# Kernel optimization log

Hardware: AMD Instinct MI355X
Metric: run time of the kernel (lower is better)

The kernel has to match this reference:

```python
import jax, jax.numpy as jnp
import numpy as np

N = 100000      # nodes
E = 1600000     # edges (avg degree 16)
IN_DIM = 256
HID = 128
EPS = 0.3


def setup_inputs() -> dict:
    key = jax.random.key(0)
    ks = jax.random.split(key, 6)
    x = jax.random.normal(ks[0], (N, IN_DIM), dtype=jnp.float32)
    # edges without self-loops (dst = src + nonzero offset mod N)
    src = jax.random.randint(ks[1], (E,), 0, N)
    off = jax.random.randint(ks[2], (E,), 1, N)
    dst = (src + off) % N
    edge_index = jnp.stack([src, dst]).astype(jnp.int32)
    # xavier_normal_ with gain=1.414 for t1 and gate
    g1 = 1.414 * np.sqrt(2.0 / (IN_DIM + HID))
    w1 = (jax.random.normal(ks[3], (HID, IN_DIM)) * g1).astype(jnp.float32)
    b1 = jnp.zeros((HID,), jnp.float32)
    gg = 1.414 * np.sqrt(2.0 / (2 * HID + 1))
    gate_w = (jax.random.normal(ks[4], (1, 2 * HID)) * gg).astype(jnp.float32)
    gate_b = jnp.zeros((1,), jnp.float32)
    return dict(x=x, edge_index=edge_index, w1=w1, b1=b1, gate_w=gate_w, gate_b=gate_b)


def reference(x, edge_index, w1, b1, gate_w, gate_b):
    src, dst = edge_index[0], edge_index[1]
    # in-degree based symmetric norm, deg clamped to >= 1
    deg = jax.ops.segment_sum(jnp.ones((E,), jnp.float32), dst, num_segments=N)
    norm = jnp.clip(deg, 1.0) ** -0.5  # [N]

    h = jax.nn.relu(x @ w1.T + b1)     # [N, HID] (dropout p=0 / eval -> identity)
    raw = h

    # gate([h_dst, h_src]) decomposed: concat @ W^T = h_dst @ w_d + h_src @ w_s
    w_d, w_s = gate_w[0, :HID], gate_w[0, HID:]
    a_dst = h @ w_d                    # [N]
    a_src = h @ w_s                    # [N]
    g = jnp.tanh(a_dst[dst] + a_src[src] + gate_b[0])   # [E] per-edge gate
    e = g * norm[dst] * norm[src]                        # [E]

    # u_mul_e + sum: gather src features, weight, scatter-add to dst
    z = jax.ops.segment_sum(h[src] * e[:, None], dst, num_segments=N)  # [N, HID]
    return EPS * raw + z
```

## Files before the change

kernel.cpp:

```cpp
#include <hip/hip_runtime.h>
#include <math.h>
#include <stdint.h>

#define N_NODES 100000
#define N_EDGES 1600000
#define IN_DIM  256
#define HID     128
#define EPS_C   0.3f

#define NPB      128
#define NBKT     782
#define NBKT_P   784
#define BCAP     3072
#define S1_CHUNK 8192
#define S1_BLOCKS 196

typedef __attribute__((ext_vector_type(8))) __bf16 bf16x8;
typedef __attribute__((ext_vector_type(4))) float  f32x4;
typedef __attribute__((ext_vector_type(8))) unsigned short ushort8;

static __device__ __forceinline__ unsigned short f2bf(float f) {
    unsigned u = __float_as_uint(f);
    unsigned r = (u + 0x7fffu + ((u >> 16) & 1u)) >> 16;
    return (unsigned short)r;
}
static __device__ __forceinline__ float bf2f(unsigned short s) {
    return __uint_as_float((unsigned)s << 16);
}
static __device__ __forceinline__ float fast_tanh(float x) {
    float e = __builtin_exp2f(x * 2.8853900817779268f);
    return 1.0f - 2.0f / (e + 1.0f);
}

__global__ __launch_bounds__(256) void convert_w1_kernel(const float* __restrict__ w1,
                                                         unsigned short* __restrict__ w1b) {
    int i = blockIdx.x * 256 + threadIdx.x;
    if (i * 4 >= HID * IN_DIM) return;
    float4 v = *(const float4*)&w1[i * 4];
    ushort4 r;
    r.x = f2bf(v.x); r.y = f2bf(v.y); r.z = f2bf(v.z); r.w = f2bf(v.w);
    *(ushort4*)&w1b[i * 4] = r;
}

__global__ __launch_bounds__(512) void partition_kernel(const int* __restrict__ src,
                                                        const int* __restrict__ dst,
                                                        int* __restrict__ gcur,
                                                        int2* __restrict__ ebuf) {
    __shared__ int hist[NBKT_P];
    __shared__ int base[NBKT_P];
    __shared__ int gpos[NBKT_P];
    __shared__ int cur[NBKT_P];
    __shared__ int seg[512];
    __shared__ int2 staged[S1_CHUNK];

    int t = threadIdx.x;
    for (int i = t; i < NBKT_P; i += 512) hist[i] = 0;
    __syncthreads();

    int base4 = blockIdx.x * (S1_CHUNK / 4);
    int rem4  = N_EDGES / 4 - base4;

    int4 sv[4], dv[4];
#pragma unroll
    for (int j = 0; j < 4; j++) {
        int i4 = j * 512 + t;
        if (i4 < rem4) {
            sv[j] = *(const int4*)&src[(base4 + i4) * 4];
            dv[j] = *(const int4*)&dst[(base4 + i4) * 4];
        } else {
            dv[j] = make_int4(-1, -1, -1, -1);
        }
    }
#pragma unroll
    for (int j = 0; j < 4; j++) {
        if (dv[j].x >= 0) {
            atomicAdd(&hist[dv[j].x >> 7], 1);
            atomicAdd(&hist[dv[j].y >> 7], 1);
            atomicAdd(&hist[dv[j].z >> 7], 1);
            atomicAdd(&hist[dv[j].w >> 7], 1);
        }
    }
    __syncthreads();

    int h0 = 0, h1 = 0;
    if (t < NBKT_P / 2) { h0 = hist[2 * t]; h1 = hist[2 * t + 1]; }
    seg[t] = h0 + h1;
    __syncthreads();
    for (int off = 1; off < 512; off <<= 1) {
        int a = (t >= off) ? seg[t - off] : 0;
        __syncthreads();
        seg[t] += a;
        __syncthreads();
    }
    if (t < NBKT_P / 2) {
        int excl = seg[t] - (h0 + h1);
        base[2 * t]     = excl;
        cur[2 * t]      = excl;
        base[2 * t + 1] = excl + h0;
        cur[2 * t + 1]  = excl + h0;
        if (h0 > 0) gpos[2 * t]     = atomicAdd(&gcur[2 * t], h0);
        if (h1 > 0) gpos[2 * t + 1] = atomicAdd(&gcur[2 * t + 1], h1);
    }
    __syncthreads();

#pragma unroll
    for (int j = 0; j < 4; j++) {
        if (dv[j].x >= 0) {
            int p;
            p = atomicAdd(&cur[dv[j].x >> 7], 1); staged[p] = make_int2(sv[j].x, dv[j].x);
            p = atomicAdd(&cur[dv[j].y >> 7], 1); staged[p] = make_int2(sv[j].y, dv[j].y);
            p = atomicAdd(&cur[dv[j].z >> 7], 1); staged[p] = make_int2(sv[j].z, dv[j].z);
            p = atomicAdd(&cur[dv[j].w >> 7], 1); staged[p] = make_int2(sv[j].w, dv[j].w);
        }
    }
    __syncthreads();

    int n = N_EDGES - base4 * 4;
    if (n > S1_CHUNK) n = S1_CHUNK;
    for (int i = t; i < n; i += 512) {
        int2 e = staged[i];
        int b = e.y >> 7;
        int off2 = gpos[b] + (i - base[b]);
        if (off2 < BCAP) ebuf[(size_t)b * BCAP + off2] = e;
    }
}

__global__ __launch_bounds__(512) void bscan_kernel(const int* __restrict__ gcur,
                                                    int* __restrict__ bstart) {
    __shared__ int s[512];
    int t = threadIdx.x;
    int a0 = 0, a1 = 0;
    if (t < NBKT_P / 2) {
        a0 = (2 * t     < NBKT) ? gcur[2 * t]     : 0;
        a1 = (2 * t + 1 < NBKT) ? gcur[2 * t + 1] : 0;
    }
    s[t] = a0 + a1;
    __syncthreads();
    for (int off = 1; off < 512; off <<= 1) {
        int a = (t >= off) ? s[t - off] : 0;
        __syncthreads();
        s[t] += a;
        __syncthreads();
    }
    if (t < NBKT_P / 2) {
        int excl = s[t] - (a0 + a1);
        if (2 * t     < NBKT) bstart[2 * t]     = excl;
        if (2 * t + 1 < NBKT) bstart[2 * t + 1] = excl + a0;
    }
}

__global__ __launch_bounds__(512) void deg_kernel(const int* __restrict__ gcur,
                                                  const int* __restrict__ bstart,
                                                  const int2* __restrict__ ebuf,
                                                  int* __restrict__ rowstart,
                                                  float* __restrict__ nrm) {
    __shared__ int dcnt[NPB];
    __shared__ int s[NPB];
    int b = blockIdx.x;
    int t = threadIdx.x;
    if (t < NPB) dcnt[t] = 0;
    __syncthreads();

    int ecnt = gcur[b];
    if (ecnt > BCAP) ecnt = BCAP;
    for (int j = t; j < ecnt; j += 512) {
        int2 e = ebuf[(size_t)b * BCAP + j];
        atomicAdd(&dcnt[e.y & (NPB - 1)], 1);
    }
    __syncthreads();

    int v = 0;
    if (t < NPB) { v = dcnt[t]; s[t] = v; }
    __syncthreads();
    for (int off = 1; off < NPB; off <<= 1) {
        int a = (t < NPB && t >= off) ? s[t - off] : 0;
        __syncthreads();
        if (t < NPB) s[t] += a;
        __syncthreads();
    }

    int nbase = b * NPB;
    int nn = N_NODES - nbase;
    if (nn > NPB) nn = NPB;
    if (t < nn) {
        rowstart[nbase + t] = bstart[b] + s[t] - v;
        nrm[nbase + t] = rsqrtf(fmaxf((float)v, 1.0f));
    }
    if (b == NBKT - 1 && t == 0) rowstart[N_NODES] = N_EDGES;
}

__global__ __launch_bounds__(256) void gemm_kernel(const float* __restrict__ x,
                                                   const unsigned short* __restrict__ w1b,
                                                   const float* __restrict__ b1,
                                                   const float* __restrict__ gw,
                                                   const float* __restrict__ nrm,
                                                   unsigned short* __restrict__ h,
                                                   float2* __restrict__ pd_pack,
                                                   float2* __restrict__ ps_pack) {
    __shared__ unsigned short As[64 * 40];
    __shared__ unsigned short Bs[128 * 40];

    int tid = threadIdx.x;
    int bm = blockIdx.x * 64;

    int wv   = tid >> 6;
    int lane = tid & 63;
    int col  = lane & 15;
    int kq   = lane >> 4;

    f32x4 acc[8];
#pragma unroll
    for (int nf = 0; nf < 8; nf++) acc[nf] = (f32x4){0.f, 0.f, 0.f, 0.f};

    int am = tid >> 2;
    int ak = (tid & 3) * 8;
    int bn = tid >> 1;
    int bk = (tid & 1) * 16;
    int agm = bm + am;

    for (int k0 = 0; k0 < IN_DIM; k0 += 32) {
        float4 a0 = {0,0,0,0}, a1 = {0,0,0,0};
        if (agm < N_NODES) {
            const float* p = &x[agm * IN_DIM + k0 + ak];
            a0 = *(const float4*)p;
            a1 = *(const float4*)(p + 4);
        }
        ushort8 av;
        av[0]=f2bf(a0.x); av[1]=f2bf(a0.y); av[2]=f2bf(a0.z); av[3]=f2bf(a0.w);
        av[4]=f2bf(a1.x); av[5]=f2bf(a1.y); av[6]=f2bf(a1.z); av[7]=f2bf(a1.w);
        ushort8 bv0 = *(const ushort8*)&w1b[bn * IN_DIM + k0 + bk];
        ushort8 bv1 = *(const ushort8*)&w1b[bn * IN_DIM + k0 + bk + 8];

        __syncthreads();
        *(ushort8*)&As[am * 40 + ak] = av;
        *(ushort8*)&Bs[bn * 40 + bk] = bv0;
        *(ushort8*)&Bs[bn * 40 + bk + 8] = bv1;
        __syncthreads();

        bf16x8 afrag = *(bf16x8*)&As[(wv * 16 + col) * 40 + kq * 8];
#pragma unroll
        for (int nf = 0; nf < 8; nf++) {
            bf16x8 bfrag = *(bf16x8*)&Bs[(nf * 16 + col) * 40 + kq * 8];
            acc[nf] = __builtin_amdgcn_mfma_f32_16x16x32_bf16(afrag, bfrag, acc[nf], 0, 0, 0);
        }
    }

    float bias[8], wd[8], wsv[8];
#pragma unroll
    for (int nf = 0; nf < 8; nf++) {
        bias[nf] = b1[nf * 16 + col];
        wd[nf]   = gw[nf * 16 + col];
        wsv[nf]  = gw[HID + nf * 16 + col];
    }
#pragma unroll
    for (int r = 0; r < 4; r++) {
        int gm = bm + wv * 16 + kq * 4 + r;
        float pd = 0.f, ps = 0.f;
        bool ok = (gm < N_NODES);
#pragma unroll
        for (int nf = 0; nf < 8; nf++) {
            float v = fmaxf(acc[nf][r] + bias[nf], 0.f);
            pd = fmaf(v, wd[nf], pd);
            ps = fmaf(v, wsv[nf], ps);
            if (ok) h[gm * HID + nf * 16 + col] = f2bf(v);
        }
#pragma unroll
        for (int m = 1; m < 16; m <<= 1) {
            pd += __shfl_xor(pd, m);
            ps += __shfl_xor(ps, m);
        }
        if (ok && col == 0) {
            float nv = nrm[gm];
            pd_pack[gm] = make_float2(pd, nv);
            ps_pack[gm] = make_float2(ps, nv);
        }
    }
}

__global__ __launch_bounds__(512) void scatter2_kernel(const int* __restrict__ gcur,
                                                       const int2* __restrict__ ebuf,
                                                       const int* __restrict__ rowstart,
                                                       const float2* __restrict__ pd_pack,
                                                       const float2* __restrict__ ps_pack,
                                                       const float* __restrict__ gb,
                                                       int2* __restrict__ epack) {
    __shared__ int    curs[NPB];
    __shared__ float2 pdl[NPB];
    int b = blockIdx.x;
    int t = threadIdx.x;
    int nbase = b * NPB;
    int nn = N_NODES - nbase;
    if (nn > NPB) nn = NPB;
    if (t < nn) {
        curs[t] = rowstart[nbase + t];
        pdl[t]  = pd_pack[nbase + t];
    }
    __syncthreads();

    int ecnt = gcur[b];
    if (ecnt > BCAP) ecnt = BCAP;
    float gbv = gb[0];
    for (int j = t; j < ecnt; j += 512) {
        int2 e = ebuf[(size_t)b * BCAP + j];
        int li = e.y & (NPB - 1);
        int pos = atomicAdd(&curs[li], 1);
        float2 pdp = pdl[li];
        float2 psp = ps_pack[e.x];
        float g = fast_tanh(pdp.x + psp.x + gbv);
        epack[pos] = make_int2(e.x, __float_as_int(g * pdp.y * psp.y));
    }
}

__global__ __launch_bounds__(256) void aggregate_kernel(const int* __restrict__ rowstart,
                                                        const int2* __restrict__ epack,
                                                        const unsigned short* __restrict__ h,
                                                        float* __restrict__ out) {
    int node = blockIdx.x * 4 + (threadIdx.x >> 6);
    if (node >= N_NODES) return;
    int lane = threadIdx.x & 63;
    int q  = lane >> 4;
    int ql = lane & 15;

    int beg = rowstart[node];
    int end = rowstart[node + 1];

    float acc[8];
#pragma unroll
    for (int t = 0; t < 8; t++) acc[t] = 0.f;

    int j = beg;
    for (; j + 8 <= end; j += 8) {
        int2 e0 = epack[j + q];
        int2 e1 = epack[j + 4 + q];
        ushort8 r0 = *(const ushort8*)&h[e0.x * HID + ql * 8];
        ushort8 r1 = *(const ushort8*)&h[e1.x * HID + ql * 8];
        float c0 = __int_as_float(e0.y);
        float c1 = __int_as_float(e1.y);
#pragma unroll
        for (int t = 0; t < 8; t++) {
            acc[t] = fmaf(c0, bf2f(r0[t]), acc[t]);
            acc[t] = fmaf(c1, bf2f(r1[t]), acc[t]);
        }
    }
    for (; j < end; j += 4) {
        bool act = (j + q) < end;
        int idx = act ? (j + q) : beg;
        int2 e = epack[idx];
        ushort8 r = *(const ushort8*)&h[e.x * HID + ql * 8];
        float c = act ? __int_as_float(e.y) : 0.f;
#pragma unroll
        for (int t = 0; t < 8; t++) acc[t] = fmaf(c, bf2f(r[t]), acc[t]);
    }
#pragma unroll
    for (int t = 0; t < 8; t++) {
        acc[t] += __shfl_xor(acc[t], 16);
        acc[t] += __shfl_xor(acc[t], 32);
    }
    if (q == 0) {
        ushort8 hd = *(const ushort8*)&h[node * HID + ql * 8];
        f32x4 o0, o1;
        o0.x = fmaf(EPS_C, bf2f(hd[0]), acc[0]);
        o0.y = fmaf(EPS_C, bf2f(hd[1]), acc[1]);
        o0.z = fmaf(EPS_C, bf2f(hd[2]), acc[2]);
        o0.w = fmaf(EPS_C, bf2f(hd[3]), acc[3]);
        o1.x = fmaf(EPS_C, bf2f(hd[4]), acc[4]);
        o1.y = fmaf(EPS_C, bf2f(hd[5]), acc[5]);
        o1.z = fmaf(EPS_C, bf2f(hd[6]), acc[6]);
        o1.w = fmaf(EPS_C, bf2f(hd[7]), acc[7]);
        __builtin_nontemporal_store(o0, (f32x4*)&out[node * HID + ql * 8]);
        __builtin_nontemporal_store(o1, (f32x4*)&out[node * HID + ql * 8 + 4]);
    }
}

extern "C" void kernel_launch(void* const* d_in, const int* in_sizes, int n_in,
                              void* d_out, int out_size, void* d_ws, size_t ws_size,
                              hipStream_t stream) {
    const float* x  = (const float*)d_in[0];
    const int*   ei = (const int*)d_in[1];
    const float* w1 = (const float*)d_in[2];
    const float* b1 = (const float*)d_in[3];
    const float* gw = (const float*)d_in[4];
    const float* gb = (const float*)d_in[5];
    float* out = (float*)d_out;

    const int* src = ei;
    const int* dst = ei + N_EDGES;

    uintptr_t base = (uintptr_t)d_ws;
    size_t off = 0;
    auto alloc = [&](size_t bytes) -> void* {
        void* p = (void*)(base + off);
        off += (bytes + 255) & ~(size_t)255;
        return p;
    };
    unsigned short* h   = (unsigned short*)alloc((size_t)N_NODES * HID * 2);
    float2* pd_pack     = (float2*)alloc((size_t)N_NODES * 8);
    float2* ps_pack     = (float2*)alloc((size_t)N_NODES * 8);
    float*  nrm         = (float*)alloc((size_t)N_NODES * 4);
    int*    rowstart    = (int*)alloc((size_t)(N_NODES + 1) * 4);
    int2*   epack       = (int2*)alloc((size_t)N_EDGES * 8);
    unsigned short* w1b = (unsigned short*)alloc((size_t)HID * IN_DIM * 2);
    int*    gcur        = (int*)alloc((size_t)NBKT * 4);
    int*    bstart      = (int*)alloc((size_t)NBKT * 4);
    int2*   ebuf        = (int2*)alloc((size_t)NBKT * BCAP * 8);

    (void)hipMemsetAsync(gcur, 0, (size_t)NBKT * 4, stream);

    convert_w1_kernel<<<(HID * IN_DIM / 4 + 255) / 256, 256, 0, stream>>>(w1, w1b);
    partition_kernel<<<S1_BLOCKS, 512, 0, stream>>>(src, dst, gcur, ebuf);
    bscan_kernel<<<1, 512, 0, stream>>>(gcur, bstart);
    deg_kernel<<<NBKT, 512, 0, stream>>>(gcur, bstart, ebuf, rowstart, nrm);
    gemm_kernel<<<(N_NODES + 63) / 64, 256, 0, stream>>>(x, w1b, b1, gw, nrm,
                                                         h, pd_pack, ps_pack);
    scatter2_kernel<<<NBKT, 512, 0, stream>>>(gcur, ebuf, rowstart,
                                              pd_pack, ps_pack, gb, epack);
    aggregate_kernel<<<(N_NODES + 3) / 4, 256, 0, stream>>>(rowstart, epack, h, out);
}
```

Baseline: 303.1 us.

## Pack bucketed edges into 32-bit words, enlarge GEMM row tile, halve partition chunk

Bucketed edges are now stored as one 32-bit word holding the source index and the local destination index, instead of an int2. This halves ebuf traffic across the partition, degree and scatter kernels. The GEMM block now covers 256 rows with four MFMA row fragments per wave, so each W1 tile in shared memory is reused across more rows, at the cost of more accumulator registers and fewer blocks. The partition chunk size is halved to launch twice as many blocks, and 64-bit index casts are added.

```diff
diff --git a/kernel.cpp b/kernel.cpp
--- a/kernel.cpp
+++ b/kernel.cpp
@@ -12,8 +12,11 @@
 #define NBKT     782
 #define NBKT_P   784
 #define BCAP     3072
-#define S1_CHUNK 8192
-#define S1_BLOCKS 196
+#define S1_CHUNK 4096
+#define S1_BLOCKS 391
+
+#define PK_SRC(p)  ((p) & 0x1FFFF)
+#define PK_LI(p)   ((p) >> 17)
 
 typedef __attribute__((ext_vector_type(8))) __bf16 bf16x8;
 typedef __attribute__((ext_vector_type(4))) float  f32x4;
@@ -45,7 +48,7 @@
 __global__ __launch_bounds__(512) void partition_kernel(const int* __restrict__ src,
                                                         const int* __restrict__ dst,
                                                         int* __restrict__ gcur,
-                                                        int2* __restrict__ ebuf) {
+                                                        int* __restrict__ ebuf) {
     __shared__ int hist[NBKT_P];
     __shared__ int base[NBKT_P];
     __shared__ int gpos[NBKT_P];
@@ -60,9 +63,9 @@
     int base4 = blockIdx.x * (S1_CHUNK / 4);
     int rem4  = N_EDGES / 4 - base4;
 
-    int4 sv[4], dv[4];
-#pragma unroll
-    for (int j = 0; j < 4; j++) {
+    int4 sv[2], dv[2];
+#pragma unroll
+    for (int j = 0; j < 2; j++) {
         int i4 = j * 512 + t;
         if (i4 < rem4) {
             sv[j] = *(const int4*)&src[(base4 + i4) * 4];
@@ -72,7 +75,7 @@
         }
     }
 #pragma unroll
-    for (int j = 0; j < 4; j++) {
+    for (int j = 0; j < 2; j++) {
         if (dv[j].x >= 0) {
             atomicAdd(&hist[dv[j].x >> 7], 1);
             atomicAdd(&hist[dv[j].y >> 7], 1);
@@ -104,7 +107,7 @@
     __syncthreads();
 
 #pragma unroll
-    for (int j = 0; j < 4; j++) {
+    for (int j = 0; j < 2; j++) {
         if (dv[j].x >= 0) {
             int p;
             p = atomicAdd(&cur[dv[j].x >> 7], 1); staged[p] = make_int2(sv[j].x, dv[j].x);
@@ -121,7 +124,7 @@
         int2 e = staged[i];
         int b = e.y >> 7;
         int off2 = gpos[b] + (i - base[b]);
-        if (off2 < BCAP) ebuf[(size_t)b * BCAP + off2] = e;
+        if (off2 < BCAP) ebuf[(size_t)b * BCAP + off2] = ((e.y & (NPB - 1)) << 17) | e.x;
     }
 }
 
@@ -151,7 +154,7 @@
 
 __global__ __launch_bounds__(512) void deg_kernel(const int* __restrict__ gcur,
                                                   const int* __restrict__ bstart,
-                                                  const int2* __restrict__ ebuf,
+                                                  const int* __restrict__ ebuf,
                                                   int* __restrict__ rowstart,
                                                   float* __restrict__ nrm) {
     __shared__ int dcnt[NPB];
@@ -163,10 +166,8 @@
 
     int ecnt = gcur[b];
     if (ecnt > BCAP) ecnt = BCAP;
-    for (int j = t; j < ecnt; j += 512) {
-        int2 e = ebuf[(size_t)b * BCAP + j];
-        atomicAdd(&dcnt[e.y & (NPB - 1)], 1);
-    }
+    for (int j = t; j < ecnt; j += 512)
+        atomicAdd(&dcnt[PK_LI(ebuf[(size_t)b * BCAP + j])], 1);
     __syncthreads();
 
     int v = 0;
@@ -197,51 +198,66 @@
                                                    unsigned short* __restrict__ h,
                                                    float2* __restrict__ pd_pack,
                                                    float2* __restrict__ ps_pack) {
-    __shared__ unsigned short As[64 * 40];
+    __shared__ unsigned short As[256 * 40];
     __shared__ unsigned short Bs[128 * 40];
 
     int tid = threadIdx.x;
-    int bm = blockIdx.x * 64;
+    int bm = blockIdx.x * 256;
 
     int wv   = tid >> 6;
     int lane = tid & 63;
     int col  = lane & 15;
     int kq   = lane >> 4;
 
-    f32x4 acc[8];
-#pragma unroll
-    for (int nf = 0; nf < 8; nf++) acc[nf] = (f32x4){0.f, 0.f, 0.f, 0.f};
+    f32x4 acc[4][8];
+#pragma unroll
+    for (int f = 0; f < 4; f++)
+#pragma unroll
+        for (int nf = 0; nf < 8; nf++) acc[f][nf] = (f32x4){0.f, 0.f, 0.f, 0.f};
 
     int am = tid >> 2;
     int ak = (tid & 3) * 8;
     int bn = tid >> 1;
     int bk = (tid & 1) * 16;
-    int agm = bm + am;
 
     for (int k0 = 0; k0 < IN_DIM; k0 += 32) {
-        float4 a0 = {0,0,0,0}, a1 = {0,0,0,0};
-        if (agm < N_NODES) {
-            const float* p = &x[agm * IN_DIM + k0 + ak];
-            a0 = *(const float4*)p;
-            a1 = *(const float4*)(p + 4);
-        }
-        ushort8 av;
-        av[0]=f2bf(a0.x); av[1]=f2bf(a0.y); av[2]=f2bf(a0.z); av[3]=f2bf(a0.w);
-        av[4]=f2bf(a1.x); av[5]=f2bf(a1.y); av[6]=f2bf(a1.z); av[7]=f2bf(a1.w);
+        ushort8 av[4];
+#pragma unroll
+        for (int sub = 0; sub < 4; sub++) {
+            int r = am + sub * 64;
+            float4 a0 = {0,0,0,0}, a1 = {0,0,0,0};
+            if (bm + r < N_NODES) {
+                const float* p = &x[(size_t)(bm + r) * IN_DIM + k0 + ak];
+                a0 = *(const float4*)p;
+                a1 = *(const float4*)(p + 4);
+            }
+            av[sub][0]=f2bf(a0.x); av[sub][1]=f2bf(a0.y);
+            av[sub][2]=f2bf(a0.z); av[sub][3]=f2bf(a0.w);
+            av[sub][4]=f2bf(a1.x); av[sub][5]=f2bf(a1.y);
+            av[sub][6]=f2bf(a1.z); av[sub][7]=f2bf(a1.w);
+        }
         ushort8 bv0 = *(const ushort8*)&w1b[bn * IN_DIM + k0 + bk];
         ushort8 bv1 = *(const ushort8*)&w1b[bn * IN_DIM + k0 + bk + 8];
 
         __syncthreads();
-        *(ushort8*)&As[am * 40 + ak] = av;
+#pragma unroll
+        for (int sub = 0; sub < 4; sub++)
+            *(ushort8*)&As[(am + sub * 64) * 40 + ak] = av[sub];
         *(ushort8*)&Bs[bn * 40 + bk] = bv0;
         *(ushort8*)&Bs[bn * 40 + bk + 8] = bv1;
         __syncthreads();
 
-        bf16x8 afrag = *(bf16x8*)&As[(wv * 16 + col) * 40 + kq * 8];
+        bf16x8 afrag[4];
+#pragma unroll
+        for (int f = 0; f < 4; f++)
+            afrag[f] = *(bf16x8*)&As[(wv * 64 + f * 16 + col) * 40 + kq * 8];
 #pragma unroll
         for (int nf = 0; nf < 8; nf++) {
             bf16x8 bfrag = *(bf16x8*)&Bs[(nf * 16 + col) * 40 + kq * 8];
-            acc[nf] = __builtin_amdgcn_mfma_f32_16x16x32_bf16(afrag, bfrag, acc[nf], 0, 0, 0);
+#pragma unroll
+            for (int f = 0; f < 4; f++)
+                acc[f][nf] = __builtin_amdgcn_mfma_f32_16x16x32_bf16(afrag[f], bfrag,
+                                                                     acc[f][nf], 0, 0, 0);
         }
     }
 
@@ -253,32 +269,35 @@
         wsv[nf]  = gw[HID + nf * 16 + col];
     }
 #pragma unroll
-    for (int r = 0; r < 4; r++) {
-        int gm = bm + wv * 16 + kq * 4 + r;
-        float pd = 0.f, ps = 0.f;
-        bool ok = (gm < N_NODES);
-#pragma unroll
-        for (int nf = 0; nf < 8; nf++) {
-            float v = fmaxf(acc[nf][r] + bias[nf], 0.f);
-            pd = fmaf(v, wd[nf], pd);
-            ps = fmaf(v, wsv[nf], ps);
-            if (ok) h[gm * HID + nf * 16 + col] = f2bf(v);
-        }
-#pragma unroll
-        for (int m = 1; m < 16; m <<= 1) {
-            pd += __shfl_xor(pd, m);
-            ps += __shfl_xor(ps, m);
-        }
-        if (ok && col == 0) {
-            float nv = nrm[gm];
-            pd_pack[gm] = make_float2(pd, nv);
-            ps_pack[gm] = make_float2(ps, nv);
+    for (int f = 0; f < 4; f++) {
+#pragma unroll
+        for (int r = 0; r < 4; r++) {
+            int gm = bm + wv * 64 + f * 16 + kq * 4 + r;
+            float pd = 0.f, ps = 0.f;
+            bool ok = (gm < N_NODES);
+#pragma unroll
+            for (int nf = 0; nf < 8; nf++) {
+                float v = fmaxf(acc[f][nf][r] + bias[nf], 0.f);
+                pd = fmaf(v, wd[nf], pd);
+                ps = fmaf(v, wsv[nf], ps);
+                if (ok) h[(size_t)gm * HID + nf * 16 + col] = f2bf(v);
+            }
+#pragma unroll
+            for (int m = 1; m < 16; m <<= 1) {
+                pd += __shfl_xor(pd, m);
+                ps += __shfl_xor(ps, m);
+            }
+            if (ok && col == 0) {
+                float nv = nrm[gm];
+                pd_pack[gm] = make_float2(pd, nv);
+                ps_pack[gm] = make_float2(ps, nv);
+            }
         }
     }
 }
 
 __global__ __launch_bounds__(512) void scatter2_kernel(const int* __restrict__ gcur,
-                                                       const int2* __restrict__ ebuf,
+                                                       const int* __restrict__ ebuf,
                                                        const int* __restrict__ rowstart,
                                                        const float2* __restrict__ pd_pack,
                                                        const float2* __restrict__ ps_pack,
@@ -301,13 +320,14 @@
     if (ecnt > BCAP) ecnt = BCAP;
     float gbv = gb[0];
     for (int j = t; j < ecnt; j += 512) {
-        int2 e = ebuf[(size_t)b * BCAP + j];
-        int li = e.y & (NPB - 1);
+        int p = ebuf[(size_t)b * BCAP + j];
+        int s  = PK_SRC(p);
+        int li = PK_LI(p);
         int pos = atomicAdd(&curs[li], 1);
         float2 pdp = pdl[li];
-        float2 psp = ps_pack[e.x];
+        float2 psp = ps_pack[s];
         float g = fast_tanh(pdp.x + psp.x + gbv);
-        epack[pos] = make_int2(e.x, __float_as_int(g * pdp.y * psp.y));
+        epack[pos] = make_int2(s, __float_as_int(g * pdp.y * psp.y));
     }
 }
 
@@ -332,8 +352,8 @@
     for (; j + 8 <= end; j += 8) {
         int2 e0 = epack[j + q];
         int2 e1 = epack[j + 4 + q];
-        ushort8 r0 = *(const ushort8*)&h[e0.x * HID + ql * 8];
-        ushort8 r1 = *(const ushort8*)&h[e1.x * HID + ql * 8];
+        ushort8 r0 = *(const ushort8*)&h[(size_t)e0.x * HID + ql * 8];
+        ushort8 r1 = *(const ushort8*)&h[(size_t)e1.x * HID + ql * 8];
         float c0 = __int_as_float(e0.y);
         float c1 = __int_as_float(e1.y);
 #pragma unroll
@@ -346,7 +366,7 @@
         bool act = (j + q) < end;
         int idx = act ? (j + q) : beg;
         int2 e = epack[idx];
-        ushort8 r = *(const ushort8*)&h[e.x * HID + ql * 8];
+        ushort8 r = *(const ushort8*)&h[(size_t)e.x * HID + ql * 8];
         float c = act ? __int_as_float(e.y) : 0.f;
 #pragma unroll
         for (int t = 0; t < 8; t++) acc[t] = fmaf(c, bf2f(r[t]), acc[t]);
@@ -357,7 +377,7 @@
         acc[t] += __shfl_xor(acc[t], 32);
     }
     if (q == 0) {
-        ushort8 hd = *(const ushort8*)&h[node * HID + ql * 8];
+        ushort8 hd = *(const ushort8*)&h[(size_t)node * HID + ql * 8];
         f32x4 o0, o1;
         o0.x = fmaf(EPS_C, bf2f(hd[0]), acc[0]);
         o0.y = fmaf(EPS_C, bf2f(hd[1]), acc[1]);
@@ -367,8 +387,8 @@
         o1.y = fmaf(EPS_C, bf2f(hd[5]), acc[5]);
         o1.z = fmaf(EPS_C, bf2f(hd[6]), acc[6]);
         o1.w = fmaf(EPS_C, bf2f(hd[7]), acc[7]);
-        __builtin_nontemporal_store(o0, (f32x4*)&out[node * HID + ql * 8]);
-        __builtin_nontemporal_store(o1, (f32x4*)&out[node * HID + ql * 8 + 4]);
+        __builtin_nontemporal_store(o0, (f32x4*)&out[(size_t)node * HID + ql * 8]);
+        __builtin_nontemporal_store(o1, (f32x4*)&out[(size_t)node * HID + ql * 8 + 4]);
     }
 }
 
@@ -402,7 +422,7 @@
     unsigned short* w1b = (unsigned short*)alloc((size_t)HID * IN_DIM * 2);
     int*    gcur        = (int*)alloc((size_t)NBKT * 4);
     int*    bstart      = (int*)alloc((size_t)NBKT * 4);
-    int2*   ebuf        = (int2*)alloc((size_t)NBKT * BCAP * 8);
+    int*    ebuf        = (int*)alloc((size_t)NBKT * BCAP * 4);
 
     (void)hipMemsetAsync(gcur, 0, (size_t)NBKT * 4, stream);
 
@@ -410,8 +430,8 @@
     partition_kernel<<<S1_BLOCKS, 512, 0, stream>>>(src, dst, gcur, ebuf);
     bscan_kernel<<<1, 512, 0, stream>>>(gcur, bstart);
     deg_kernel<<<NBKT, 512, 0, stream>>>(gcur, bstart, ebuf, rowstart, nrm);
-    gemm_kernel<<<(N_NODES + 63) / 64, 256, 0, stream>>>(x, w1b, b1, gw, nrm,
-                                                         h, pd_pack, ps_pack);
+    gemm_kernel<<<(N_NODES + 255) / 256, 256, 0, stream>>>(x, w1b, b1, gw, nrm,
+                                                           h, pd_pack, ps_pack);
     scatter2_kernel<<<NBKT, 512, 0, stream>>>(gcur, ebuf, rowstart,
                                               pd_pack, ps_pack, gb, epack);
     aggregate_kernel<<<(N_NODES + 3) / 4, 256, 0, stream>>>(rowstart, epack, h, out);
```

After: 313.9 us. 3.6% more time.
